# Optimization experiments

Measured on AMD Instinct MI355X. Metric: run time of the kernel, lower is better.

The kernel has to match this reference:

```python
import jax, jax.numpy as jnp
import numpy as np

B = 1024        # number of graphs in batch
NNODES = 64     # nodes per graph
NODE = 4        # node feature size
EDGEF = 2       # edge feature size
HID = 32        # hidden_dim
NFACT = 3       # num_factories
NE = 1024       # edges per graph (self.edges list length)


def setup_inputs() -> dict:
    key = jax.random.key(0)
    ks = jax.random.split(key, 12)
    rng = np.random.default_rng(1)
    # per-graph edge list (self.edges in the torch module)
    edges = rng.integers(0, NNODES, size=(NE, 2))
    edges_src = jnp.asarray(edges[:, 0], dtype=jnp.int32)   # [NE]
    edges_dst = jnp.asarray(edges[:, 1], dtype=jnp.int32)   # [NE]
    # batched edge_index for EdgeConv: same per-graph edges offset by b*NNODES
    offs = np.arange(B, dtype=np.int64)[:, None] * NNODES   # [B,1]
    ei_src = (edges[:, 0][None, :] + offs).reshape(-1)
    ei_dst = (edges[:, 1][None, :] + offs).reshape(-1)
    edge_index = jnp.asarray(np.stack([ei_src, ei_dst], 0), dtype=jnp.int32)  # [2, B*NE]

    N = B * NNODES
    E = B * NE
    x = jax.random.normal(ks[0], (N, NODE), dtype=jnp.float32)
    edge_attr = jax.random.normal(ks[1], (E, EDGEF), dtype=jnp.float32)
    action = jax.random.uniform(ks[2], (B, NE + NFACT), dtype=jnp.float32)

    s = 0.1
    W1 = jax.random.normal(ks[3], (2 * NODE + EDGEF, HID), dtype=jnp.float32) * s
    b1 = jnp.zeros((HID,), jnp.float32)
    W2 = jax.random.normal(ks[4], (HID, HID), dtype=jnp.float32) * s
    b2 = jnp.zeros((HID,), jnp.float32)
    D = (NODE + HID) * 2 + 1  # 73
    Wl = jax.random.normal(ks[5], (D, HID), dtype=jnp.float32) * s
    bl = jnp.zeros((HID,), jnp.float32)
    Wv = jax.random.normal(ks[6], (HID, 1), dtype=jnp.float32) * s
    bv = jnp.zeros((1,), jnp.float32)

    return {"x": x, "edge_index": edge_index, "edge_attr": edge_attr,
            "action": action, "edges_src": edges_src, "edges_dst": edges_dst,
            "W1": W1, "b1": b1, "W2": W2, "b2": b2,
            "Wl": Wl, "bl": bl, "Wv": Wv, "bv": bv}


def reference(x, edge_index, edge_attr, action, edges_src, edges_dst,
              W1, b1, W2, b2, Wl, bl, Wv, bv):
    N = x.shape[0]
    src = edge_index[0]  # flow='target_to_source': x_i = x[src], aggregate at src
    dst = edge_index[1]
    # EdgeConv message: MLP(cat[x_i, x_j, edge_attr])
    tmp = jnp.concatenate([x[src], x[dst], edge_attr], axis=1)  # [E, 10]
    msg = jax.nn.relu(tmp @ W1 + b1) @ W2 + b2                  # [E, HID]
    x_pp = jax.ops.segment_sum(msg, src, num_segments=N)        # scatter-add
    # concat node feats with conv output, split into graphs
    h = jnp.concatenate([x, x_pp], axis=1).reshape(B, NNODES, NODE + HID)  # [B,NN,36]
    # gather per-edge endpoint features
    ef = jnp.concatenate([h[:, edges_src], h[:, edges_dst]], axis=2)       # [B,NE,72]
    # factory features: last NFACT nodes duplicated
    pf = jnp.concatenate([h[:, -NFACT:], h[:, -NFACT:]], axis=-1)          # [B,NF,72]
    feats = jnp.concatenate([ef, pf], axis=1)                               # [B,NE+NF,72]
    concat = jnp.concatenate([feats, action[..., None]], axis=-1)           # [B,NE+NF,73]
    hidden = jax.nn.relu(concat @ Wl + bl)                                  # [B,NE+NF,HID]
    v = hidden @ Wv + bv                                                    # [B,NE+NF,1]
    return jnp.sum(v, axis=1).squeeze(-1)                                   # [B]
```

## Files before the change

kernel.cpp:

```cpp
#include <hip/hip_runtime.h>

#define NNODES 64
#define HID 32
#define NFACT 3
#define NE 1024
#define NROWS (NE + NFACT)
#define TPB 256
#define STR 36
#define MAXTILES 128

#define WS_DEG  64
#define WS_TN   128
#define WS_PE   256

typedef short bf16x8 __attribute__((ext_vector_type(8)));
typedef float f32x4  __attribute__((ext_vector_type(4)));
typedef float f32x16 __attribute__((ext_vector_type(16)));

__device__ __forceinline__ unsigned pack_bf2(float lo, float hi) {
    unsigned ul = __builtin_bit_cast(unsigned, lo);
    unsigned uh = __builtin_bit_cast(unsigned, hi);
    ul += 0x7fffu + ((ul >> 16) & 1u);
    uh += 0x7fffu + ((uh >> 16) & 1u);
    return (ul >> 16) | (uh & 0xffff0000u);
}
__device__ __forceinline__ short f2bf(float f) {
    unsigned u = __builtin_bit_cast(unsigned, f);
    u += 0x7fffu + ((u >> 16) & 1u);
    return (short)(u >> 16);
}
__device__ __forceinline__ float4 fma4(float a, float4 w, float4 c) {
    c.x = fmaf(a, w.x, c.x); c.y = fmaf(a, w.y, c.y);
    c.z = fmaf(a, w.z, c.z); c.w = fmaf(a, w.w, c.w);
    return c;
}

__global__ __launch_bounds__(TPB) void build_csr(const int* __restrict__ es,
                                                 const int* __restrict__ ed,
                                                 int* __restrict__ ws) {
    __shared__ int sdeg[NNODES], soff[NNODES], scnt[NNODES];
    const int tid = threadIdx.x;
    if (tid < NNODES) { sdeg[tid] = 0; scnt[tid] = 0; }
    if (tid < MAXTILES) ws[WS_TN + tid] = 0;
#pragma unroll 1
    for (int i = tid; i < MAXTILES * 16; i += TPB) ws[WS_PE + i] = 0xFFF;
    __syncthreads();
#pragma unroll 1
    for (int e = tid; e < NE; e += TPB) atomicAdd(&sdeg[es[e]], 1);
    __syncthreads();
    if (tid < NNODES) {
        const int cnt = (sdeg[tid] + 15) >> 4;
        int scan = cnt;
#pragma unroll
        for (int o = 1; o < 64; o <<= 1) {
            const int v = __shfl_up(scan, o);
            if (tid >= o) scan += v;
        }
        soff[tid] = scan - cnt;
        ws[WS_DEG + tid] = sdeg[tid];
        if (tid == NNODES - 1) ws[0] = scan;
    }
    __syncthreads();
    if (tid < NNODES) {
        const int base = soff[tid], cnt = (sdeg[tid] + 15) >> 4;
        const int padv = 0xFFF | (tid << 18);
#pragma unroll 1
        for (int j = 0; j < cnt; j++) {
            ws[WS_TN + base + j] = tid;
#pragma unroll 1
            for (int s = 0; s < 16; s++) ws[WS_PE + (base + j) * 16 + s] = padv;
        }
    }
    __syncthreads();
#pragma unroll 1
    for (int e = tid; e < NE; e += TPB) {
        const int n = es[e];
        const int idx = atomicAdd(&scnt[n], 1);
        ws[WS_PE + soff[n] * 16 + idx] = e | (ed[e] << 12) | (n << 18);
    }
}

__global__ __launch_bounds__(TPB, 4) void critic_fused(
    const float* __restrict__ x,
    const float* __restrict__ edge_attr,
    const float* __restrict__ action,
    const int*   __restrict__ es,
    const int*   __restrict__ ed,
    const float* __restrict__ W1,
    const float* __restrict__ b1,
    const float* __restrict__ W2,
    const float* __restrict__ b2,
    const float* __restrict__ Wl,
    const float* __restrict__ bl,
    const float* __restrict__ Wv,
    const float* __restrict__ bv,
    const int*   __restrict__ csr,
    float* __restrict__ out)
{
    const int b    = blockIdx.x;
    const int tid  = threadIdx.x;
    const int lane = tid & 63;
    const int wv   = tid >> 6;
    const int quad = lane >> 4;
    const int m16  = lane & 15;
    const int kh   = quad * 8;

    __shared__ float4 xs4[NNODES];
    __shared__ float  xpp[NNODES * STR];
    __shared__ float  qp0[NNODES * STR];
    __shared__ float  qp1[NNODES * STR];
    __shared__ float  W1s[10 * HID];
    __shared__ float  b1s[HID];
    __shared__ float  wred[TPB / 64];

    if (tid < NNODES) xs4[tid] = ((const float4*)x)[b * NNODES + tid];
    if (tid < 80) ((float4*)W1s)[tid] = ((const float4*)W1)[tid];
    if (tid < HID) b1s[tid] = b1[tid];
#pragma unroll 1
    for (int i = tid; i < NNODES * STR; i += TPB) xpp[i] = 0.0f;
    __syncthreads();

    const int n  = tid & 63;
    const int k0 = (tid >> 6) * 8;

    {
        const float4 xv = xs4[n];
        const float4* b1v = (const float4*)&b1s[k0];
        float4 q1a = b1v[0], q1b = b1v[1];
        float4 q2a = make_float4(0.f, 0.f, 0.f, 0.f), q2b = q2a;
#pragma unroll 1
        for (int i = 0; i < 4; i++) {
            const float xi = (i == 0) ? xv.x : (i == 1) ? xv.y : (i == 2) ? xv.z : xv.w;
            const float4* wa = (const float4*)&W1s[i * HID + k0];
            const float4* wb = (const float4*)&W1s[(4 + i) * HID + k0];
            q1a = fma4(xi, wa[0], q1a); q1b = fma4(xi, wa[1], q1b);
            q2a = fma4(xi, wb[0], q2a); q2b = fma4(xi, wb[1], q2b);
        }
        float4* q1w = (float4*)&qp0[n * STR + k0];
        float4* q2w = (float4*)&qp1[n * STR + k0];
        q1w[0] = q1a; q1w[1] = q1b;
        q2w[0] = q2a; q2w[1] = q2b;
    }
    __syncthreads();

    {
        const float2* ea2 = (const float2*)edge_attr + (size_t)b * NE;
        const int NW  = TPB / 64;
        const int klo = (lane >> 5) * 8;
        const int n32 = lane & 31;

        const float4* w8l = (const float4*)&W1s[8 * HID + klo];
        const float4* w8h = (const float4*)&W1s[8 * HID + 16 + klo];
        const float4* w9l = (const float4*)&W1s[9 * HID + klo];
        const float4* w9h = (const float4*)&W1s[9 * HID + 16 + klo];
        const float4 w8a = w8l[0], w8b = w8l[1], w8c = w8h[0], w8d = w8h[1];
        const float4 w9a = w9l[0], w9b = w9l[1], w9c = w9h[0], w9d = w9h[1];

        bf16x8 bfA, bfB;
#pragma unroll
        for (int j = 0; j < 8; j++) {
            bfA[j] = f2bf(W2[(klo + j) * HID + n32]);
            bfB[j] = f2bf(W2[(16 + klo + j) * HID + n32]);
        }

        const int  ntiles = csr[0];
        const int  np     = (ntiles + 1) >> 1;
        const int* tn  = csr + WS_TN;
        const int* pep = csr + WS_PE;

#pragma unroll 1
        for (int p = wv; p < np; p += NW) {
            const int raw = pep[p * 32 + n32];
            const int tA  = tn[2 * p];
            const int tB  = tn[2 * p + 1];
            const int e    = raw & 0xFFF;
            const bool pad = (e == 0xFFF);
            const int d0   = (raw >> 12) & 63;
            const int nd   = (raw >> 18) & 63;
            const float2 ea = ea2[pad ? 0 : e];

            const float4* A1 = (const float4*)&qp0[nd * STR + klo];
            const float4* A2 = (const float4*)&qp0[nd * STR + 16 + klo];
            const float4* G1 = (const float4*)&qp1[d0 * STR + klo];
            const float4* G2 = (const float4*)&qp1[d0 * STR + 16 + klo];
            const float4 a0 = A1[0], a1 = A1[1], a2 = A2[0], a3 = A2[1];
            const float4 g0 = G1[0], g1 = G1[1], g2 = G2[0], g3 = G2[1];

            const float hx0 = fmaxf(a0.x + g0.x + ea.x * w8a.x + ea.y * w9a.x, 0.f);
            const float hx1 = fmaxf(a0.y + g0.y + ea.x * w8a.y + ea.y * w9a.y, 0.f);
            const float hx2 = fmaxf(a0.z + g0.z + ea.x * w8a.z + ea.y * w9a.z, 0.f);
            const float hx3 = fmaxf(a0.w + g0.w + ea.x * w8a.w + ea.y * w9a.w, 0.f);
            const float hx4 = fmaxf(a1.x + g1.x + ea.x * w8b.x + ea.y * w9b.x, 0.f);
            const float hx5 = fmaxf(a1.y + g1.y + ea.x * w8b.y + ea.y * w9b.y, 0.f);
            const float hx6 = fmaxf(a1.z + g1.z + ea.x * w8b.z + ea.y * w9b.z, 0.f);
            const float hx7 = fmaxf(a1.w + g1.w + ea.x * w8b.w + ea.y * w9b.w, 0.f);
            const float hy0 = fmaxf(a2.x + g2.x + ea.x * w8c.x + ea.y * w9c.x, 0.f);
            const float hy1 = fmaxf(a2.y + g2.y + ea.x * w8c.y + ea.y * w9c.y, 0.f);
            const float hy2 = fmaxf(a2.z + g2.z + ea.x * w8c.z + ea.y * w9c.z, 0.f);
            const float hy3 = fmaxf(a2.w + g2.w + ea.x * w8c.w + ea.y * w9c.w, 0.f);
            const float hy4 = fmaxf(a3.x + g3.x + ea.x * w8d.x + ea.y * w9d.x, 0.f);
            const float hy5 = fmaxf(a3.y + g3.y + ea.x * w8d.y + ea.y * w9d.y, 0.f);
            const float hy6 = fmaxf(a3.z + g3.z + ea.x * w8d.z + ea.y * w9d.z, 0.f);
            const float hy7 = fmaxf(a3.w + g3.w + ea.x * w8d.w + ea.y * w9d.w, 0.f);

            uint4 pkA, pkB;
            pkA.x = pad ? 0u : pack_bf2(hx0, hx1);
            pkA.y = pad ? 0u : pack_bf2(hx2, hx3);
            pkA.z = pad ? 0u : pack_bf2(hx4, hx5);
            pkA.w = pad ? 0u : pack_bf2(hx6, hx7);
            pkB.x = pad ? 0u : pack_bf2(hy0, hy1);
            pkB.y = pad ? 0u : pack_bf2(hy2, hy3);
            pkB.z = pad ? 0u : pack_bf2(hy4, hy5);
            pkB.w = pad ? 0u : pack_bf2(hy6, hy7);
            const bf16x8 afA = __builtin_bit_cast(bf16x8, pkA);
            const bf16x8 afB = __builtin_bit_cast(bf16x8, pkB);

            f32x16 c;
#pragma unroll
            for (int j = 0; j < 16; j++) c[j] = 0.0f;
            c = __builtin_amdgcn_mfma_f32_32x32x16_bf16(afA, bfA, c, 0, 0, 0);
            c = __builtin_amdgcn_mfma_f32_32x32x16_bf16(afB, bfB, c, 0, 0, 0);

            float sA = ((c[0] + c[1]) + (c[2] + c[3])) + ((c[4] + c[5]) + (c[6] + c[7]));
            float sB = ((c[8] + c[9]) + (c[10] + c[11])) + ((c[12] + c[13]) + (c[14] + c[15]));
            sA += __shfl_xor(sA, 32);
            sB += __shfl_xor(sB, 32);
            const int   nst = (lane < 32) ? tA : tB;
            const float sv  = (lane < 32) ? sA : sB;
            atomicAdd(&xpp[nst * STR + n32], sv);
        }
    }
    __syncthreads();

    bf16x8 bP1a, bP1b, bP2a, bP2b;
#pragma unroll
    for (int j = 0; j < 8; j++) {
        bP1a[j] = f2bf(Wl[(4 + kh + j) * HID + m16]);
        bP1b[j] = f2bf(Wl[(4 + kh + j) * HID + 16 + m16]);
        bP2a[j] = f2bf(Wl[(40 + kh + j) * HID + m16]);
        bP2b[j] = f2bf(Wl[(40 + kh + j) * HID + 16 + m16]);
    }
    float wx1a[4], wx1b[4], wx2a[4], wx2b[4];
#pragma unroll
    for (int i = 0; i < 4; i++) {
        wx1a[i] = Wl[i * HID + m16];
        wx1b[i] = Wl[i * HID + 16 + m16];
        wx2a[i] = Wl[(36 + i) * HID + m16];
        wx2b[i] = Wl[(36 + i) * HID + 16 + m16];
    }
    const float blca = bl[m16], blcb = bl[16 + m16];
    float b2k[8];
#pragma unroll
    for (int j = 0; j < 8; j++) b2k[j] = b2[kh + j];
    const int   mrow = wv * 16 + m16;
    const float dn   = (float)csr[WS_DEG + mrow];

    {
        const float4* xr = (const float4*)&xpp[mrow * STR + kh];
        float4 x0 = xr[0], x1 = xr[1];
        x0.x = fmaf(dn, b2k[0], x0.x); x0.y = fmaf(dn, b2k[1], x0.y);
        x0.z = fmaf(dn, b2k[2], x0.z); x0.w = fmaf(dn, b2k[3], x0.w);
        x1.x = fmaf(dn, b2k[4], x1.x); x1.y = fmaf(dn, b2k[5], x1.y);
        x1.z = fmaf(dn, b2k[6], x1.z); x1.w = fmaf(dn, b2k[7], x1.w);
        uint4 packed;
        packed.x = pack_bf2(x0.x, x0.y);
        packed.y = pack_bf2(x0.z, x0.w);
        packed.z = pack_bf2(x1.x, x1.y);
        packed.w = pack_bf2(x1.z, x1.w);
        const bf16x8 af = __builtin_bit_cast(bf16x8, packed);

        f32x4 c1a, c1b, c2a, c2b;
#pragma unroll
        for (int r = 0; r < 4; r++) {
            const float4 xv = xs4[wv * 16 + quad * 4 + r];
            float a0 = blca, a1 = blcb, a2 = 0.f, a3 = 0.f;
#pragma unroll
            for (int i = 0; i < 4; i++) {
                const float xi = (i == 0) ? xv.x : (i == 1) ? xv.y : (i == 2) ? xv.z : xv.w;
                a0 = fmaf(xi, wx1a[i], a0);
                a1 = fmaf(xi, wx1b[i], a1);
                a2 = fmaf(xi, wx2a[i], a2);
                a3 = fmaf(xi, wx2b[i], a3);
            }
            c1a[r] = a0; c1b[r] = a1; c2a[r] = a2; c2b[r] = a3;
        }
        c1a = __builtin_amdgcn_mfma_f32_16x16x32_bf16(af, bP1a, c1a, 0, 0, 0);
        c1b = __builtin_amdgcn_mfma_f32_16x16x32_bf16(af, bP1b, c1b, 0, 0, 0);
        c2a = __builtin_amdgcn_mfma_f32_16x16x32_bf16(af, bP2a, c2a, 0, 0, 0);
        c2b = __builtin_amdgcn_mfma_f32_16x16x32_bf16(af, bP2b, c2b, 0, 0, 0);

#pragma unroll
        for (int r = 0; r < 4; r++) {
            const int row = wv * 16 + quad * 4 + r;
            qp0[row * STR + m16]      = c1a[r];
            qp0[row * STR + 16 + m16] = c1b[r];
            qp1[row * STR + m16]      = c2a[r];
            qp1[row * STR + 16 + m16] = c2b[r];
        }
    }
    __syncthreads();

    float vsum = 0.0f;
    {
        const float* actb = action + (size_t)b * NROWS;
        const float bvv = bv[0];
        const float* Wl72 = Wl + 72 * HID;
#pragma unroll 1
        for (int i = 0; i < 4; i++) {
            const int r = tid + i * TPB;
            const int na = es[r], nb = ed[r];
            const float a = actb[r];
            const float4* p1v = (const float4*)&qp0[na * STR];
            const float4* p2v = (const float4*)&qp1[nb * STR];
            float v0 = bvv, v1 = 0.0f;
#pragma unroll 1
            for (int q = 0; q < 8; q += 2) {
                const float4 pa0 = p1v[q],     pb0 = p2v[q];
                const float4 pa1 = p1v[q + 1], pb1 = p2v[q + 1];
                const int k = q * 4;
                v0 += fmaxf(pa0.x + pb0.x + a * Wl72[k+0], 0.f) * Wv[k+0];
                v1 += fmaxf(pa0.y + pb0.y + a * Wl72[k+1], 0.f) * Wv[k+1];
                v0 += fmaxf(pa0.z + pb0.z + a * Wl72[k+2], 0.f) * Wv[k+2];
                v1 += fmaxf(pa0.w + pb0.w + a * Wl72[k+3], 0.f) * Wv[k+3];
                v0 += fmaxf(pa1.x + pb1.x + a * Wl72[k+4], 0.f) * Wv[k+4];
                v1 += fmaxf(pa1.y + pb1.y + a * Wl72[k+5], 0.f) * Wv[k+5];
                v0 += fmaxf(pa1.z + pb1.z + a * Wl72[k+6], 0.f) * Wv[k+6];
                v1 += fmaxf(pa1.w + pb1.w + a * Wl72[k+7], 0.f) * Wv[k+7];
            }
            vsum += v0 + v1;
        }
        if (tid < NFACT) {
            const int r = NE + tid;
            const int na = NNODES - NFACT + tid;
            const float a = actb[r];
            const float4* p1v = (const float4*)&qp0[na * STR];
            const float4* p2v = (const float4*)&qp1[na * STR];
            float v = bvv;
#pragma unroll 1
            for (int q = 0; q < 8; q++) {
                const float4 pa = p1v[q], pb = p2v[q];
                const int k = q * 4;
                v += fmaxf(pa.x + pb.x + a * Wl72[k+0], 0.f) * Wv[k+0];
                v += fmaxf(pa.y + pb.y + a * Wl72[k+1], 0.f) * Wv[k+1];
                v += fmaxf(pa.z + pb.z + a * Wl72[k+2], 0.f) * Wv[k+2];
                v += fmaxf(pa.w + pb.w + a * Wl72[k+3], 0.f) * Wv[k+3];
            }
            vsum += v;
        }
    }

#pragma unroll
    for (int off = 32; off > 0; off >>= 1)
        vsum += __shfl_down(vsum, off, 64);
    if ((tid & 63) == 0) wred[tid >> 6] = vsum;
    __syncthreads();
    if (tid == 0) {
        float t = 0.0f;
#pragma unroll
        for (int w = 0; w < TPB / 64; w++) t += wred[w];
        out[b] = t;
    }
}

extern "C" void kernel_launch(void* const* d_in, const int* in_sizes, int n_in,
                              void* d_out, int out_size, void* d_ws, size_t ws_size,
                              hipStream_t stream) {
    const float* x         = (const float*)d_in[0];
    const float* edge_attr = (const float*)d_in[2];
    const float* action    = (const float*)d_in[3];
    const int*   es        = (const int*)d_in[4];
    const int*   ed        = (const int*)d_in[5];
    const float* W1        = (const float*)d_in[6];
    const float* b1        = (const float*)d_in[7];
    const float* W2        = (const float*)d_in[8];
    const float* b2        = (const float*)d_in[9];
    const float* Wl        = (const float*)d_in[10];
    const float* bl        = (const float*)d_in[11];
    const float* Wv        = (const float*)d_in[12];
    const float* bv        = (const float*)d_in[13];
    float* out = (float*)d_out;
    int*   ws  = (int*)d_ws;

    build_csr<<<dim3(1), dim3(TPB), 0, stream>>>(es, ed, ws);
    critic_fused<<<dim3(out_size), dim3(TPB), 0, stream>>>(
        x, edge_attr, action, es, ed, W1, b1, W2, b2, Wl, bl, Wv, bv, ws, out);
}
```

Measured before the change: 132.1 us.

## Build per-graph edge CSR inside the fused kernel and drop separate launch

Removes the single-block build_csr kernel and rebuilds the edge tiling (degrees, tile offsets, packed edge list) in shared memory within every block of critic_fused. Edge indices are loaded once into registers and reused for the final edge-feature stage. This eliminates a serialized one-block launch and the global workspace reads. In exchange, each block repeats the redundant CSR work, adds barriers and uses more LDS, which may affect occupancy.

```diff
diff --git a/kernel.cpp b/kernel.cpp
--- a/kernel.cpp
+++ b/kernel.cpp
@@ -8,10 +8,7 @@
 #define TPB 256
 #define STR 36
 #define MAXTILES 128
-
-#define WS_DEG  64
-#define WS_TN   128
-#define WS_PE   256
+#define EPT (NE / TPB)
 
 typedef short bf16x8 __attribute__((ext_vector_type(8)));
 typedef float f32x4  __attribute__((ext_vector_type(4)));
@@ -33,51 +30,6 @@
     c.x = fmaf(a, w.x, c.x); c.y = fmaf(a, w.y, c.y);
     c.z = fmaf(a, w.z, c.z); c.w = fmaf(a, w.w, c.w);
     return c;
-}
-
-__global__ __launch_bounds__(TPB) void build_csr(const int* __restrict__ es,
-                                                 const int* __restrict__ ed,
-                                                 int* __restrict__ ws) {
-    __shared__ int sdeg[NNODES], soff[NNODES], scnt[NNODES];
-    const int tid = threadIdx.x;
-    if (tid < NNODES) { sdeg[tid] = 0; scnt[tid] = 0; }
-    if (tid < MAXTILES) ws[WS_TN + tid] = 0;
-#pragma unroll 1
-    for (int i = tid; i < MAXTILES * 16; i += TPB) ws[WS_PE + i] = 0xFFF;
-    __syncthreads();
-#pragma unroll 1
-    for (int e = tid; e < NE; e += TPB) atomicAdd(&sdeg[es[e]], 1);
-    __syncthreads();
-    if (tid < NNODES) {
-        const int cnt = (sdeg[tid] + 15) >> 4;
-        int scan = cnt;
-#pragma unroll
-        for (int o = 1; o < 64; o <<= 1) {
-            const int v = __shfl_up(scan, o);
-            if (tid >= o) scan += v;
-        }
-        soff[tid] = scan - cnt;
-        ws[WS_DEG + tid] = sdeg[tid];
-        if (tid == NNODES - 1) ws[0] = scan;
-    }
-    __syncthreads();
-    if (tid < NNODES) {
-        const int base = soff[tid], cnt = (sdeg[tid] + 15) >> 4;
-        const int padv = 0xFFF | (tid << 18);
-#pragma unroll 1
-        for (int j = 0; j < cnt; j++) {
-            ws[WS_TN + base + j] = tid;
-#pragma unroll 1
-            for (int s = 0; s < 16; s++) ws[WS_PE + (base + j) * 16 + s] = padv;
-        }
-    }
-    __syncthreads();
-#pragma unroll 1
-    for (int e = tid; e < NE; e += TPB) {
-        const int n = es[e];
-        const int idx = atomicAdd(&scnt[n], 1);
-        ws[WS_PE + soff[n] * 16 + idx] = e | (ed[e] << 12) | (n << 18);
-    }
 }
 
 __global__ __launch_bounds__(TPB, 4) void critic_fused(
@@ -94,7 +46,6 @@
     const float* __restrict__ bl,
     const float* __restrict__ Wv,
     const float* __restrict__ bv,
-    const int*   __restrict__ csr,
     float* __restrict__ out)
 {
     const int b    = blockIdx.x;
@@ -112,18 +63,33 @@
     __shared__ float  W1s[10 * HID];
     __shared__ float  b1s[HID];
     __shared__ float  wred[TPB / 64];
-
-    if (tid < NNODES) xs4[tid] = ((const float4*)x)[b * NNODES + tid];
+    __shared__ int    sdeg[NNODES], soff[NNODES], scnt[NNODES];
+    __shared__ int    tns[MAXTILES];
+    __shared__ int    pep[MAXTILES * 16];
+    __shared__ int    snt;
+
+    if (tid < NNODES) { xs4[tid] = ((const float4*)x)[b * NNODES + tid]; sdeg[tid] = 0; scnt[tid] = 0; }
     if (tid < 80) ((float4*)W1s)[tid] = ((const float4*)W1)[tid];
     if (tid < HID) b1s[tid] = b1[tid];
+    if (tid < MAXTILES) tns[tid] = 0;
+#pragma unroll
+    for (int i = 0; i < MAXTILES * 16 / TPB; i++) pep[tid + i * TPB] = 0xFFF;
 #pragma unroll 1
     for (int i = tid; i < NNODES * STR; i += TPB) xpp[i] = 0.0f;
-    __syncthreads();
-
-    const int n  = tid & 63;
-    const int k0 = (tid >> 6) * 8;
-
+
+    int ces[EPT], ced[EPT];
+#pragma unroll
+    for (int i = 0; i < EPT; i++) {
+        ces[i] = es[tid + i * TPB];
+        ced[i] = ed[tid + i * TPB];
+    }
+    __syncthreads();
+
+#pragma unroll
+    for (int i = 0; i < EPT; i++) atomicAdd(&sdeg[ces[i]], 1);
     {
+        const int n  = lane;
+        const int k0 = wv * 8;
         const float4 xv = xs4[n];
         const float4* b1v = (const float4*)&b1s[k0];
         float4 q1a = b1v[0], q1b = b1v[1];
@@ -143,6 +109,39 @@
     }
     __syncthreads();
 
+    if (tid < NNODES) {
+        const int cnt = (sdeg[tid] + 15) >> 4;
+        int scan = cnt;
+#pragma unroll
+        for (int o = 1; o < 64; o <<= 1) {
+            const int v = __shfl_up(scan, o);
+            if (tid >= o) scan += v;
+        }
+        soff[tid] = scan - cnt;
+        if (tid == NNODES - 1) snt = scan;
+    }
+    __syncthreads();
+
+    if (tid < NNODES) {
+        const int base = soff[tid], cnt = (sdeg[tid] + 15) >> 4;
+        const int padv = 0xFFF | (tid << 18);
+#pragma unroll 1
+        for (int j = 0; j < cnt; j++) {
+            tns[base + j] = tid;
+#pragma unroll 1
+            for (int s = 0; s < 16; s++) pep[(base + j) * 16 + s] = padv;
+        }
+    }
+    __syncthreads();
+
+#pragma unroll
+    for (int i = 0; i < EPT; i++) {
+        const int n = ces[i];
+        const int idx = atomicAdd(&scnt[n], 1);
+        pep[soff[n] * 16 + idx] = (tid + i * TPB) | (ced[i] << 12) | (n << 18);
+    }
+    __syncthreads();
+
     {
         const float2* ea2 = (const float2*)edge_attr + (size_t)b * NE;
         const int NW  = TPB / 64;
@@ -163,16 +162,13 @@
             bfB[j] = f2bf(W2[(16 + klo + j) * HID + n32]);
         }
 
-        const int  ntiles = csr[0];
-        const int  np     = (ntiles + 1) >> 1;
-        const int* tn  = csr + WS_TN;
-        const int* pep = csr + WS_PE;
+        const int np = (snt + 1) >> 1;
 
 #pragma unroll 1
         for (int p = wv; p < np; p += NW) {
             const int raw = pep[p * 32 + n32];
-            const int tA  = tn[2 * p];
-            const int tB  = tn[2 * p + 1];
+            const int tA  = tns[2 * p];
+            const int tB  = tns[2 * p + 1];
             const int e    = raw & 0xFFF;
             const bool pad = (e == 0xFFF);
             const int d0   = (raw >> 12) & 63;
@@ -253,7 +249,7 @@
 #pragma unroll
     for (int j = 0; j < 8; j++) b2k[j] = b2[kh + j];
     const int   mrow = wv * 16 + m16;
-    const float dn   = (float)csr[WS_DEG + mrow];
+    const float dn   = (float)sdeg[mrow];
 
     {
         const float4* xr = (const float4*)&xpp[mrow * STR + kh];
@@ -307,9 +303,8 @@
         const float* Wl72 = Wl + 72 * HID;
 #pragma unroll 1
         for (int i = 0; i < 4; i++) {
-            const int r = tid + i * TPB;
-            const int na = es[r], nb = ed[r];
-            const float a = actb[r];
+            const int na = ces[i], nb = ced[i];
+            const float a = actb[tid + i * TPB];
             const float4* p1v = (const float4*)&qp0[na * STR];
             const float4* p2v = (const float4*)&qp1[nb * STR];
             float v0 = bvv, v1 = 0.0f;
@@ -379,9 +374,7 @@
     const float* Wv        = (const float*)d_in[12];
     const float* bv        = (const float*)d_in[13];
     float* out = (float*)d_out;
-    int*   ws  = (int*)d_ws;
-
-    build_csr<<<dim3(1), dim3(TPB), 0, stream>>>(es, ed, ws);
+
     critic_fused<<<dim3(out_size), dim3(TPB), 0, stream>>>(
-        x, edge_attr, action, es, ed, W1, b1, W2, b2, Wl, bl, Wv, bv, ws, out);
-}
+        x, edge_attr, action, es, ed, W1, b1, W2, b2, Wl, bl, Wv, bv, out);
+}
```

Result: faster. 128.8 us (-2.5%).
